# Performance work log

Hardware: AMD Instinct MI355X
Metric: run time of the kernel (lower is better)

Reference implementation:

```python
import jax, jax.numpy as jnp
import numpy as np

B, S, D = 1, 1500, 1280
H = 20
HD = D // H
FFN = 5120
EPS = 1e-5


def _layer_norm(x, w, b):
    # manual LN as in the NPU graph: mean/var/div, eps=1e-5
    mean = jnp.mean(x, axis=-1, keepdims=True)
    var = jnp.mean((x - mean) ** 2, axis=-1, keepdims=True)
    return w * ((x - mean) / jnp.sqrt(var + EPS)) + b


def setup_inputs() -> dict:
    key = jax.random.key(0)
    ks = jax.random.split(key, 16)
    r = lambda k, shp, s=1.0: jax.random.normal(k, shp, dtype=jnp.float32) * s
    return {
        "x": r(ks[0], (B, S, D)),
        "ln1_w": jax.random.uniform(ks[1], (D,), dtype=jnp.float32),
        "ln1_b": r(ks[2], (D,), 0.02),
        "ln2_w": jax.random.uniform(ks[3], (D,), dtype=jnp.float32),
        "ln2_b": r(ks[4], (D,), 0.02),
        "wq": r(ks[5], (D, D), 0.02),
        "q_bias": r(ks[6], (D,), 0.02),
        "wk": r(ks[7], (D, D), 0.02),
        "wv": r(ks[8], (D, D), 0.02),
        "v_bias": r(ks[9], (D,), 0.02),
        "wo": r(ks[10], (D, D), 0.02),
        "out_bias": r(ks[11], (D,), 0.02),
        "w_fc1": r(ks[12], (FFN, D), 0.02),
        "fc1_bias": r(ks[13], (FFN,), 0.02),
        "w_fc2": r(ks[14], (D, FFN), 0.02),
        "fc2_bias": r(ks[15], (D,), 0.02),
    }


def reference(x, ln1_w, ln1_b, ln2_w, ln2_b, wq, q_bias, wk, wv, v_bias,
              wo, out_bias, w_fc1, fc1_bias, w_fc2, fc2_bias):
    scaling = HD ** -0.5
    residual = x
    h = _layer_norm(x.reshape(B * S, D), ln1_w, ln1_b)

    # self-attention (k_proj has no bias, as in Whisper)
    q = (h @ wq.T + q_bias) * scaling            # [S, D]
    k = h @ wk.T
    v = h @ wv.T + v_bias
    q = q.reshape(S, H, HD).transpose(1, 0, 2)   # [H, S, HD]
    k = k.reshape(S, H, HD).transpose(1, 0, 2)
    v = v.reshape(S, H, HD).transpose(1, 0, 2)

    attn = jnp.einsum('hqd,hkd->hqk', q, k)      # [H, S, S]
    attn = jax.nn.softmax(attn, axis=-1)
    ctx = jnp.einsum('hqk,hkd->hqd', attn, v)    # [H, S, HD]
    ctx = ctx.transpose(1, 0, 2).reshape(S, D)
    attn_out = ctx @ wo.T + out_bias

    h = residual + attn_out.reshape(B, S, D)

    residual = h
    h2 = _layer_norm(h.reshape(B * S, D), ln2_w, ln2_b)
    h2 = jax.nn.gelu(h2 @ w_fc1.T + fc1_bias, approximate=False)
    h2 = h2 @ w_fc2.T + fc2_bias
    return residual + h2.reshape(B, S, D)
```

## Files before the change

### kernel.cpp

```cpp
#include <hip/hip_runtime.h>
#include <math.h>

typedef unsigned short u16;
typedef __attribute__((ext_vector_type(8))) short bf16x8;
typedef __attribute__((ext_vector_type(4))) float f32x4;

#define S_VALID 1500
#define S_PAD   1536
#define DMODEL  1280
#define NHEAD   20
#define HDIM    64
#define FFND    5120
#define NKV_TILES 47

__device__ __forceinline__ u16 f2bf(float f) {
  union { float f; unsigned u; } v; v.f = f;
  unsigned r = v.u + 0x7fffu + ((v.u >> 16) & 1u);
  return (u16)(r >> 16);
}

template <int N>
__device__ __forceinline__ void wait_vmcnt() {
  if constexpr (N == 8)      asm volatile("s_waitcnt vmcnt(8)"  ::: "memory");
  else if constexpr (N == 6) asm volatile("s_waitcnt vmcnt(6)"  ::: "memory");
  else if constexpr (N == 4) asm volatile("s_waitcnt vmcnt(4)"  ::: "memory");
  else                       asm volatile("s_waitcnt vmcnt(0)"  ::: "memory");
}

__global__ void k_cvt4(const float* __restrict__ s0, const float* __restrict__ s1,
                       const float* __restrict__ s2, const float* __restrict__ s3,
                       u16* __restrict__ d0, u16* __restrict__ d1,
                       u16* __restrict__ d2, u16* __restrict__ d3, int n) {
  const float* in = (blockIdx.y == 0) ? s0 : (blockIdx.y == 1) ? s1 : (blockIdx.y == 2) ? s2 : s3;
  u16* out = (blockIdx.y == 0) ? d0 : (blockIdx.y == 1) ? d1 : (blockIdx.y == 2) ? d2 : d3;
  int i = (blockIdx.x * 256 + threadIdx.x) * 4;
  if (i >= n) return;
  float4 f = *(const float4*)(in + i);
  union { u16 s[4]; uint2 v; } o;
  o.s[0] = f2bf(f.x); o.s[1] = f2bf(f.y); o.s[2] = f2bf(f.z); o.s[3] = f2bf(f.w);
  *(uint2*)(out + i) = o.v;
}
__global__ void k_cvt2(const float* __restrict__ s0, const float* __restrict__ s1,
                       u16* __restrict__ d0, u16* __restrict__ d1, int n) {
  const float* in = (blockIdx.y == 0) ? s0 : s1;
  u16* out = (blockIdx.y == 0) ? d0 : d1;
  int i = (blockIdx.x * 256 + threadIdx.x) * 4;
  if (i >= n) return;
  float4 f = *(const float4*)(in + i);
  union { u16 s[4]; uint2 v; } o;
  o.s[0] = f2bf(f.x); o.s[1] = f2bf(f.y); o.s[2] = f2bf(f.z); o.s[3] = f2bf(f.w);
  *(uint2*)(out + i) = o.v;
}

__global__ __launch_bounds__(256) void k_ln(const float* __restrict__ x,
                                            const float* __restrict__ w,
                                            const float* __restrict__ b,
                                            u16* __restrict__ out, int rows_valid) {
  int r = blockIdx.x;
  int t = threadIdx.x;
  if (r >= rows_valid) {
    for (int i = t; i < DMODEL; i += 256) out[r * DMODEL + i] = 0;
    return;
  }
  const float* xr = x + (size_t)r * DMODEL;
  float vals[5]; float s = 0.f, ss = 0.f;
#pragma unroll
  for (int j = 0; j < 5; ++j) {
    float v = xr[t + j * 256]; vals[j] = v; s += v; ss += v * v;
  }
#pragma unroll
  for (int m = 1; m < 64; m <<= 1) { s += __shfl_xor(s, m); ss += __shfl_xor(ss, m); }
  __shared__ float ps[4], pss[4];
  int lane = t & 63, wv = t >> 6;
  if (lane == 0) { ps[wv] = s; pss[wv] = ss; }
  __syncthreads();
  s = ps[0] + ps[1] + ps[2] + ps[3];
  ss = pss[0] + pss[1] + pss[2] + pss[3];
  float mean = s * (1.f / DMODEL);
  float var = ss * (1.f / DMODEL) - mean * mean;
  float rstd = rsqrtf(var + 1e-5f);
#pragma unroll
  for (int j = 0; j < 5; ++j) {
    int i = t + j * 256;
    out[r * DMODEL + i] = f2bf(w[i] * ((vals[j] - mean) * rstd) + b[i]);
  }
}

struct EpiParams {
  const float* bias;
  const float* resid;
  float* outf;
  u16* outb;
  u16* q; u16* k; u16* vt;
  const float* qb; const float* vb;
  int mvalid;
};

template <int ROWS>
__device__ __forceinline__ void stage_tile(const u16* __restrict__ g, int ld,
                                           u16* lds, int t) {
  constexpr int ITERS = ROWS * 128 / (256 * 16);
#pragma unroll
  for (int i = 0; i < ITERS; ++i) {
    int off = i * 4096 + t * 16;
    int row = off >> 7;
    int sp  = (off >> 4) & 7;
    int s   = sp ^ (row & 7);
    const u16* gp = g + row * ld + s * 8;
    u16* lp = lds + i * 2048 + ((t >> 6) << 9);
    __builtin_amdgcn_global_load_lds((const __attribute__((address_space(1))) void*)gp,
                                     (__attribute__((address_space(3))) void*)lp,
                                     16, 0, 0);
  }
}

__device__ __forceinline__ bf16x8 ld_frag(const u16* lds, int row, int kk, int lane) {
  int slot = kk * 4 + (lane >> 4);
  int sp = slot ^ (row & 7);
  return *(const bf16x8*)(lds + row * 64 + sp * 8);
}

template <int BM, int BN, int EPI>
__global__ __launch_bounds__(256) void k_gemm(const u16* __restrict__ A,
                                              const u16* __restrict__ B,
                                              int N, int K, int lda, int ldb,
                                              EpiParams ep) {
  constexpr int FM = BM / 32, FN = BN / 32;
  constexpr int LOADS = (BM + BN) / 32;
  __shared__ __align__(128) u16 lds_a[2][BM * 64];
  __shared__ __align__(128) u16 lds_b[2][BN * 64];
  const int t = threadIdx.x, lane = t & 63, wid = t >> 6;
  const int wm = wid >> 1, wn = wid & 1;

  unsigned nwg = gridDim.x * gridDim.y;
  unsigned bid = blockIdx.y * gridDim.x + blockIdx.x;
  unsigned cpx = nwg >> 3;
  bid = (bid & 7u) * cpx + (bid >> 3);
  const int bm0 = (bid % gridDim.x) * BM, bn0 = (bid / gridDim.x) * BN;

  const int l15 = lane & 15, g4 = lane >> 4;

  f32x4 acc[FM][FN] = {};
  const size_t zk = (EPI == 4) ? (size_t)blockIdx.z * K : 0;
  const u16* Ab = A + (size_t)bm0 * lda + zk;
  const u16* Bb = B + (size_t)bn0 * ldb + zk;

  auto stage = [&](int kt, int buf) {
    stage_tile<BM>(Ab + kt * 64, lda, &lds_a[buf][0], t);
    stage_tile<BN>(Bb + kt * 64, ldb, &lds_b[buf][0], t);
  };

  const int NT = K >> 6;
  stage(0, 0);
  int buf = 0;

  for (int kt = 0; kt < NT; ++kt) {
    if (kt + 1 < NT) {
      stage(kt + 1, buf ^ 1);
      wait_vmcnt<LOADS>();
    } else {
      wait_vmcnt<0>();
    }
    __builtin_amdgcn_s_barrier();
    const u16* la = &lds_a[buf][0];
    const u16* lb = &lds_b[buf][0];
#pragma unroll
    for (int kk = 0; kk < 2; ++kk) {
      bf16x8 af[FM], bfr[FN];
#pragma unroll
      for (int i = 0; i < FM; ++i) af[i]  = ld_frag(la, wm * (BM / 2) + i * 16 + l15, kk, lane);
#pragma unroll
      for (int j = 0; j < FN; ++j) bfr[j] = ld_frag(lb, wn * (BN / 2) + j * 16 + l15, kk, lane);
#pragma unroll
      for (int i = 0; i < FM; ++i)
#pragma unroll
        for (int j = 0; j < FN; ++j)
          acc[i][j] = __builtin_amdgcn_mfma_f32_16x16x32_bf16(af[i], bfr[j], acc[i][j], 0, 0, 0);
    }
    __builtin_amdgcn_s_barrier();
    buf ^= 1;
  }

#pragma unroll
  for (int i = 0; i < FM; ++i)
#pragma unroll
    for (int j = 0; j < FN; ++j) {
      int n = bn0 + wn * (BN / 2) + j * 16 + l15;
      int mbase = bm0 + wm * (BM / 2) + i * 16 + g4 * 4;
      if constexpr (EPI == 0) {
        if (n >= 2 * DMODEL) {
          int nn = n - 2 * DMODEL;
          union { u16 s[4]; uint2 v2; } pk;
#pragma unroll
          for (int r = 0; r < 4; ++r) {
            int m = mbase + r;
            float val = (m < ep.mvalid) ? (acc[i][j][r] + ep.vb[nn]) : 0.f;
            pk.s[r] = f2bf(val);
          }
          *(uint2*)(ep.vt + (size_t)nn * S_PAD + mbase) = pk.v2;
        } else {
#pragma unroll
          for (int r = 0; r < 4; ++r) {
            int m = mbase + r;
            float v = acc[i][j][r];
            if (n < DMODEL) {
              float val = (m < ep.mvalid) ? (v + ep.qb[n]) * 0.125f : 0.f;
              ep.q[m * DMODEL + n] = f2bf(val);
            } else {
              int nn = n - DMODEL;
              ep.k[m * DMODEL + nn] = f2bf(m < ep.mvalid ? v : 0.f);
            }
          }
        }
      } else {
#pragma unroll
        for (int r = 0; r < 4; ++r) {
          int m = mbase + r;
          float v = acc[i][j][r];
          if constexpr (EPI == 2) {
            float xx = v + ep.bias[n];
            float gg = 0.5f * xx * (1.f + erff(xx * 0.70710678118f));
            ep.outb[(size_t)m * N + n] = f2bf(gg);
          } else if constexpr (EPI == 4) {
            ep.outf[((size_t)blockIdx.z * S_PAD + m) * DMODEL + n] = v;
          }
        }
      }
    }
}

__global__ __launch_bounds__(256) void k_red(const float* __restrict__ p,
                                             const float* __restrict__ bias,
                                             const float* __restrict__ resid,
                                             float* __restrict__ out) {
  int idx = blockIdx.x * 256 + threadIdx.x;
  if (idx >= S_VALID * (DMODEL / 4)) return;
  int m = idx / (DMODEL / 4), n4 = (idx % (DMODEL / 4)) * 4;
  float4 a  = *(const float4*)(p + (size_t)m * DMODEL + n4);
  float4 b  = *(const float4*)(p + ((size_t)S_PAD + m) * DMODEL + n4);
  float4 rs = *(const float4*)(resid + (size_t)m * DMODEL + n4);
  float4 bb = *(const float4*)(bias + n4);
  float4 o;
  o.x = a.x + b.x + rs.x + bb.x;
  o.y = a.y + b.y + rs.y + bb.y;
  o.z = a.z + b.z + rs.z + bb.z;
  o.w = a.w + b.w + rs.w + bb.w;
  *(float4*)(out + (size_t)m * DMODEL + n4) = o;
}

__global__ __launch_bounds__(256) void k_attn(const u16* __restrict__ q,
                                              const u16* __restrict__ k,
                                              const u16* __restrict__ vt,
                                              u16* __restrict__ ctx) {
  __shared__ __align__(128) u16 kls[2][32 * 64];
  __shared__ __align__(128) u16 vls[2][32 * 64];
  const int t = threadIdx.x;
  const int lane = t & 63, wid = t >> 6;
  const int h = blockIdx.y;
  const int qbase = blockIdx.x * 64 + wid * 16;
  const int l15 = lane & 15, g = lane >> 4;

  const int srow = t >> 3;
  const int psl  = t & 7;
  const int slog = psl ^ (srow & 7);
  const int kperm = 8 * ((srow & 15) >> 2) + (srow & 3) + 4 * (srow >> 4);
  const int vd    = 2 * srow + (slog >> 2);
  const int vkoff = (slog & 3) * 8;
  const u16* ksrc = k + (size_t)kperm * DMODEL + h * HDIM + slog * 8;
  const u16* vsrc = vt + (size_t)(h * HDIM + vd) * S_PAD + vkoff;
  const int wbase = (t >> 6) << 9;

  bf16x8 qf[2];
#pragma unroll
  for (int half = 0; half < 2; ++half)
    qf[half] = *(const bf16x8*)(q + (qbase + l15) * DMODEL + h * HDIM + half * 32 + g * 8);

  auto stage = [&](int tt, int buf) {
    __builtin_amdgcn_global_load_lds(
        (const __attribute__((address_space(1))) void*)(ksrc + (size_t)tt * 32 * DMODEL),
        (__attribute__((address_space(3))) void*)(&kls[buf][0] + wbase), 16, 0, 0);
    __builtin_amdgcn_global_load_lds(
        (const __attribute__((address_space(1))) void*)(vsrc + tt * 32),
        (__attribute__((address_space(3))) void*)(&vls[buf][0] + wbase), 16, 0, 0);
  };

  stage(0, 0);
  __syncthreads();
  int buf = 0;

  float Mx = -1e30f, L = 0.f;
  f32x4 c[4] = {};

  for (int tt = 0; tt < NKV_TILES; ++tt) {
    if (tt + 1 < NKV_TILES) stage(tt + 1, buf ^ 1);
    const u16* kb = &kls[buf][0];
    const u16* vbL = &vls[buf][0];

    f32x4 sc[2];
#pragma unroll
    for (int s = 0; s < 2; ++s) {
      int row = 16 * s + l15;
      bf16x8 ka0 = *(const bf16x8*)(kb + row * 64 + ((g)     ^ (row & 7)) * 8);
      bf16x8 ka1 = *(const bf16x8*)(kb + row * 64 + ((4 + g) ^ (row & 7)) * 8);
      f32x4 z = {};
      z = __builtin_amdgcn_mfma_f32_16x16x32_bf16(ka0, qf[0], z, 0, 0, 0);
      z = __builtin_amdgcn_mfma_f32_16x16x32_bf16(ka1, qf[1], z, 0, 0, 0);
      sc[s] = z;
    }
    float pm = -1e30f;
#pragma unroll
    for (int s = 0; s < 2; ++s)
#pragma unroll
      for (int r = 0; r < 4; ++r) {
        int kg = tt * 32 + 8 * g + 4 * s + r;
        float v = (kg < S_VALID) ? sc[s][r] : -1e30f;
        sc[s][r] = v;
        pm = fmaxf(pm, v);
      }
    pm = fmaxf(pm, __shfl_xor(pm, 16));
    pm = fmaxf(pm, __shfl_xor(pm, 32));
    float Mn = fmaxf(Mx, pm);
    float fac = __expf(Mx - Mn);
    float p[8]; float rs = 0.f;
#pragma unroll
    for (int s = 0; s < 2; ++s)
#pragma unroll
      for (int r = 0; r < 4; ++r) {
        float e = __expf(sc[s][r] - Mn);
        p[4 * s + r] = e; rs += e;
      }
    rs += __shfl_xor(rs, 16);
    rs += __shfl_xor(rs, 32);
    L = L * fac + rs; Mx = Mn;

    float facr[4];
#pragma unroll
    for (int r = 0; r < 4; ++r) facr[r] = __shfl(fac, g * 20 + r);
#pragma unroll
    for (int ch = 0; ch < 4; ++ch)
#pragma unroll
      for (int r = 0; r < 4; ++r) c[ch][r] *= facr[r];

    bf16x8 pa;
#pragma unroll
    for (int j = 0; j < 8; ++j) pa[j] = (short)f2bf(p[j]);
#pragma unroll
    for (int ch = 0; ch < 4; ++ch) {
      int R = 8 * ch + (l15 >> 1);
      int sl = (l15 & 1) * 4 + g;
      bf16x8 vbf = *(const bf16x8*)(vbL + R * 64 + (sl ^ (R & 7)) * 8);
      c[ch] = __builtin_amdgcn_mfma_f32_16x16x32_bf16(pa, vbf, c[ch], 0, 0, 0);
    }
    __syncthreads();
    buf ^= 1;
  }

  float linv = 1.f / L;
  float lr[4];
#pragma unroll
  for (int r = 0; r < 4; ++r) lr[r] = __shfl(linv, g * 20 + r);
#pragma unroll
  for (int ch = 0; ch < 4; ++ch)
#pragma unroll
    for (int r = 0; r < 4; ++r) {
      int m = qbase + g * 4 + r;
      ctx[m * DMODEL + h * HDIM + ch * 16 + l15] = f2bf(c[ch][r] * lr[r]);
    }
}

extern "C" void kernel_launch(void* const* d_in, const int* in_sizes, int n_in,
                              void* d_out, int out_size, void* d_ws, size_t ws_size,
                              hipStream_t stream) {
  const float* x    = (const float*)d_in[0];
  const float* ln1w = (const float*)d_in[1];
  const float* ln1b = (const float*)d_in[2];
  const float* ln2w = (const float*)d_in[3];
  const float* ln2b = (const float*)d_in[4];
  const float* wq   = (const float*)d_in[5];
  const float* qb   = (const float*)d_in[6];
  const float* wk   = (const float*)d_in[7];
  const float* wv   = (const float*)d_in[8];
  const float* vb   = (const float*)d_in[9];
  const float* wo   = (const float*)d_in[10];
  const float* ob   = (const float*)d_in[11];
  const float* wfc1 = (const float*)d_in[12];
  const float* fb1  = (const float*)d_in[13];
  const float* wfc2 = (const float*)d_in[14];
  const float* fb2  = (const float*)d_in[15];

  char* ws = (char*)d_ws;
  size_t off = 0;
  auto alloc = [&](size_t bytes) {
    void* p = ws + off; off += (bytes + 255) & ~(size_t)255; return p;
  };
  u16*   w_qkv = (u16*)alloc((size_t)3 * DMODEL * DMODEL * 2);
  u16*   w_o   = (u16*)alloc((size_t)DMODEL * DMODEL * 2);
  u16*   w_f1  = (u16*)alloc((size_t)FFND * DMODEL * 2);
  u16*   w_f2  = (u16*)alloc((size_t)DMODEL * FFND * 2);
  u16*   hbuf  = (u16*)alloc((size_t)S_PAD * DMODEL * 2);
  u16*   qbuf  = (u16*)alloc((size_t)S_PAD * DMODEL * 2);
  u16*   kbuf  = (u16*)alloc((size_t)S_PAD * DMODEL * 2);
  u16*   vtb   = (u16*)alloc((size_t)DMODEL * S_PAD * 2);
  u16*   ctxb  = (u16*)alloc((size_t)S_PAD * DMODEL * 2);
  float* res2  = (float*)alloc((size_t)S_PAD * DMODEL * 4);
  u16*   h2buf = (u16*)alloc((size_t)S_PAD * DMODEL * 2);
  u16*   gbuf  = (u16*)alloc((size_t)S_PAD * FFND * 2);
  float* skp   = (float*)hbuf;
  (void)ws_size; (void)n_in; (void)in_sizes; (void)out_size;

  const int nDD = DMODEL * DMODEL;
  const int nF  = FFND * DMODEL;
  k_cvt4<<<dim3(nDD / 1024, 4), 256, 0, stream>>>(
      wq, wk, wv, wo, w_qkv, w_qkv + (size_t)nDD, w_qkv + (size_t)2 * nDD, w_o, nDD);
  k_cvt2<<<dim3(nF / 1024, 2), 256, 0, stream>>>(wfc1, wfc2, w_f1, w_f2, nF);

  k_ln<<<S_PAD, 256, 0, stream>>>(x, ln1w, ln1b, hbuf, S_VALID);

  {
    EpiParams ep = {};
    ep.q = qbuf; ep.k = kbuf; ep.vt = vtb; ep.qb = qb; ep.vb = vb; ep.mvalid = S_VALID;
    k_gemm<64, 64, 0><<<dim3(S_PAD / 64, 3 * DMODEL / 64), 256, 0, stream>>>(
        hbuf, w_qkv, 3 * DMODEL, DMODEL, DMODEL, DMODEL, ep);
  }

  k_attn<<<dim3(S_PAD / 64, NHEAD), 256, 0, stream>>>(qbuf, kbuf, vtb, ctxb);

  {
    EpiParams ep = {};
    ep.outf = skp; ep.mvalid = S_VALID;
    k_gemm<64, 64, 4><<<dim3(S_PAD / 64, DMODEL / 64, 2), 256, 0, stream>>>(
        ctxb, w_o, DMODEL, DMODEL / 2, DMODEL, DMODEL, ep);
  }
  k_red<<<(S_VALID * (DMODEL / 4) + 255) / 256, 256, 0, stream>>>(
      skp, ob, x, res2);

  k_ln<<<S_PAD, 256, 0, stream>>>(res2, ln2w, ln2b, h2buf, S_VALID);

  {
    EpiParams ep = {};
    ep.bias = fb1; ep.outb = gbuf; ep.mvalid = S_VALID;
    k_gemm<64, 64, 2><<<dim3(S_PAD / 64, FFND / 64), 256, 0, stream>>>(
        h2buf, w_f1, FFND, DMODEL, DMODEL, DMODEL, ep);
  }

  {
    EpiParams ep = {};
    ep.outf = skp; ep.mvalid = S_VALID;
    k_gemm<64, 64, 4><<<dim3(S_PAD / 64, DMODEL / 64, 2), 256, 0, stream>>>(
        gbuf, w_f2, DMODEL, FFND / 2, FFND, FFND, ep);
  }
  k_red<<<(S_VALID * (DMODEL / 4) + 255) / 256, 256, 0, stream>>>(
      skp, fb2, res2, (float*)d_out);
}
```

Measured before the change: 208.6 us.

## Split attention keys in two halves with a combine kernel and 64-key tiles

The attention kernel now splits the key range into two halves of 768 across a third grid dimension, doubling the block count from 480 to 960 so the GPU's compute units are better filled. Each half writes unnormalized bf16 partial outputs plus per-row max and sum, and a new combine kernel merges them with rescaling. Each iteration now processes 64 keys from two 32-key LDS subtiles, and the barrier uses explicit vmcnt waits with s_barrier in place of __syncthreads. In exchange it adds an extra launch, extra global traffic for the partials, and bf16 rounding of the unnormalized partials, and it reuses the res2 buffer as scratch.

```diff
diff --git a/kernel.cpp b/kernel.cpp
--- a/kernel.cpp
+++ b/kernel.cpp
@@ -11,12 +11,16 @@
 #define NHEAD   20
 #define HDIM    64
 #define FFND    5120
-#define NKV_TILES 47
+#define ZKEYS   768
+#define NSPLIT_TILES 12
 
 __device__ __forceinline__ u16 f2bf(float f) {
   union { float f; unsigned u; } v; v.f = f;
   unsigned r = v.u + 0x7fffu + ((v.u >> 16) & 1u);
   return (u16)(r >> 16);
+}
+__device__ __forceinline__ float bf2f(u16 h) {
+  union { unsigned u; float f; } v; v.u = ((unsigned)h) << 16; return v.f;
 }
 
 template <int N>
@@ -251,12 +255,15 @@
 __global__ __launch_bounds__(256) void k_attn(const u16* __restrict__ q,
                                               const u16* __restrict__ k,
                                               const u16* __restrict__ vt,
-                                              u16* __restrict__ ctx) {
-  __shared__ __align__(128) u16 kls[2][32 * 64];
-  __shared__ __align__(128) u16 vls[2][32 * 64];
+                                              u16* __restrict__ o0,
+                                              u16* __restrict__ o1,
+                                              float2* __restrict__ ml) {
+  __shared__ __align__(128) u16 kls[2][2][2048];
+  __shared__ __align__(128) u16 vls[2][2][2048];
   const int t = threadIdx.x;
   const int lane = t & 63, wid = t >> 6;
-  const int h = blockIdx.y;
+  const int h = blockIdx.y, z = blockIdx.z;
+  const int zb = z * ZKEYS;
   const int qbase = blockIdx.x * 64 + wid * 16;
   const int l15 = lane & 15, g = lane >> 4;
 
@@ -266,8 +273,8 @@
   const int kperm = 8 * ((srow & 15) >> 2) + (srow & 3) + 4 * (srow >> 4);
   const int vd    = 2 * srow + (slog >> 2);
   const int vkoff = (slog & 3) * 8;
-  const u16* ksrc = k + (size_t)kperm * DMODEL + h * HDIM + slog * 8;
-  const u16* vsrc = vt + (size_t)(h * HDIM + vd) * S_PAD + vkoff;
+  const u16* kbasep = k + (size_t)kperm * DMODEL + h * HDIM + slog * 8;
+  const u16* vbasep = vt + (size_t)(h * HDIM + vd) * S_PAD + vkoff;
   const int wbase = (t >> 6) << 9;
 
   bf16x8 qf[2];
@@ -276,59 +283,73 @@
     qf[half] = *(const bf16x8*)(q + (qbase + l15) * DMODEL + h * HDIM + half * 32 + g * 8);
 
   auto stage = [&](int tt, int buf) {
-    __builtin_amdgcn_global_load_lds(
-        (const __attribute__((address_space(1))) void*)(ksrc + (size_t)tt * 32 * DMODEL),
-        (__attribute__((address_space(3))) void*)(&kls[buf][0] + wbase), 16, 0, 0);
-    __builtin_amdgcn_global_load_lds(
-        (const __attribute__((address_space(1))) void*)(vsrc + tt * 32),
-        (__attribute__((address_space(3))) void*)(&vls[buf][0] + wbase), 16, 0, 0);
+#pragma unroll
+    for (int u = 0; u < 2; ++u) {
+      int keyoff = zb + tt * 64 + u * 32;
+      __builtin_amdgcn_global_load_lds(
+          (const __attribute__((address_space(1))) void*)(kbasep + (size_t)keyoff * DMODEL),
+          (__attribute__((address_space(3))) void*)(&kls[buf][u][0] + wbase), 16, 0, 0);
+      __builtin_amdgcn_global_load_lds(
+          (const __attribute__((address_space(1))) void*)(vbasep + keyoff),
+          (__attribute__((address_space(3))) void*)(&vls[buf][u][0] + wbase), 16, 0, 0);
+    }
   };
 
   stage(0, 0);
-  __syncthreads();
   int buf = 0;
 
   float Mx = -1e30f, L = 0.f;
   f32x4 c[4] = {};
 
-  for (int tt = 0; tt < NKV_TILES; ++tt) {
-    if (tt + 1 < NKV_TILES) stage(tt + 1, buf ^ 1);
-    const u16* kb = &kls[buf][0];
-    const u16* vbL = &vls[buf][0];
-
-    f32x4 sc[2];
-#pragma unroll
-    for (int s = 0; s < 2; ++s) {
-      int row = 16 * s + l15;
-      bf16x8 ka0 = *(const bf16x8*)(kb + row * 64 + ((g)     ^ (row & 7)) * 8);
-      bf16x8 ka1 = *(const bf16x8*)(kb + row * 64 + ((4 + g) ^ (row & 7)) * 8);
-      f32x4 z = {};
-      z = __builtin_amdgcn_mfma_f32_16x16x32_bf16(ka0, qf[0], z, 0, 0, 0);
-      z = __builtin_amdgcn_mfma_f32_16x16x32_bf16(ka1, qf[1], z, 0, 0, 0);
-      sc[s] = z;
-    }
+  for (int tt = 0; tt < NSPLIT_TILES; ++tt) {
+    if (tt + 1 < NSPLIT_TILES) {
+      stage(tt + 1, buf ^ 1);
+      wait_vmcnt<4>();
+    } else {
+      wait_vmcnt<0>();
+    }
+    __builtin_amdgcn_s_barrier();
+
+    f32x4 sc[2][2];
+#pragma unroll
+    for (int u = 0; u < 2; ++u)
+#pragma unroll
+      for (int s = 0; s < 2; ++s) {
+        int row = 16 * s + l15;
+        const u16* kb = &kls[buf][u][0];
+        bf16x8 ka0 = *(const bf16x8*)(kb + row * 64 + ((g)     ^ (row & 7)) * 8);
+        bf16x8 ka1 = *(const bf16x8*)(kb + row * 64 + ((4 + g) ^ (row & 7)) * 8);
+        f32x4 zz = {};
+        zz = __builtin_amdgcn_mfma_f32_16x16x32_bf16(ka0, qf[0], zz, 0, 0, 0);
+        zz = __builtin_amdgcn_mfma_f32_16x16x32_bf16(ka1, qf[1], zz, 0, 0, 0);
+        sc[u][s] = zz;
+      }
     float pm = -1e30f;
 #pragma unroll
-    for (int s = 0; s < 2; ++s)
-#pragma unroll
-      for (int r = 0; r < 4; ++r) {
-        int kg = tt * 32 + 8 * g + 4 * s + r;
-        float v = (kg < S_VALID) ? sc[s][r] : -1e30f;
-        sc[s][r] = v;
-        pm = fmaxf(pm, v);
-      }
+    for (int u = 0; u < 2; ++u)
+#pragma unroll
+      for (int s = 0; s < 2; ++s)
+#pragma unroll
+        for (int r = 0; r < 4; ++r) {
+          int kg = zb + tt * 64 + u * 32 + 8 * g + 4 * s + r;
+          float v = (kg < S_VALID) ? sc[u][s][r] : -1e30f;
+          sc[u][s][r] = v;
+          pm = fmaxf(pm, v);
+        }
     pm = fmaxf(pm, __shfl_xor(pm, 16));
     pm = fmaxf(pm, __shfl_xor(pm, 32));
     float Mn = fmaxf(Mx, pm);
     float fac = __expf(Mx - Mn);
-    float p[8]; float rs = 0.f;
-#pragma unroll
-    for (int s = 0; s < 2; ++s)
-#pragma unroll
-      for (int r = 0; r < 4; ++r) {
-        float e = __expf(sc[s][r] - Mn);
-        p[4 * s + r] = e; rs += e;
-      }
+    float p[2][8]; float rs = 0.f;
+#pragma unroll
+    for (int u = 0; u < 2; ++u)
+#pragma unroll
+      for (int s = 0; s < 2; ++s)
+#pragma unroll
+        for (int r = 0; r < 4; ++r) {
+          float e = __expf(sc[u][s][r] - Mn);
+          p[u][4 * s + r] = e; rs += e;
+        }
     rs += __shfl_xor(rs, 16);
     rs += __shfl_xor(rs, 32);
     L = L * fac + rs; Mx = Mn;
@@ -341,31 +362,57 @@
 #pragma unroll
       for (int r = 0; r < 4; ++r) c[ch][r] *= facr[r];
 
-    bf16x8 pa;
-#pragma unroll
-    for (int j = 0; j < 8; ++j) pa[j] = (short)f2bf(p[j]);
+    bf16x8 pa[2];
+#pragma unroll
+    for (int u = 0; u < 2; ++u)
+#pragma unroll
+      for (int j = 0; j < 8; ++j) pa[u][j] = (short)f2bf(p[u][j]);
 #pragma unroll
     for (int ch = 0; ch < 4; ++ch) {
       int R = 8 * ch + (l15 >> 1);
       int sl = (l15 & 1) * 4 + g;
-      bf16x8 vbf = *(const bf16x8*)(vbL + R * 64 + (sl ^ (R & 7)) * 8);
-      c[ch] = __builtin_amdgcn_mfma_f32_16x16x32_bf16(pa, vbf, c[ch], 0, 0, 0);
-    }
-    __syncthreads();
+#pragma unroll
+      for (int u = 0; u < 2; ++u) {
+        bf16x8 vbf = *(const bf16x8*)(&vls[buf][u][0] + R * 64 + (sl ^ (R & 7)) * 8);
+        c[ch] = __builtin_amdgcn_mfma_f32_16x16x32_bf16(pa[u], vbf, c[ch], 0, 0, 0);
+      }
+    }
+    __builtin_amdgcn_s_barrier();
     buf ^= 1;
   }
 
-  float linv = 1.f / L;
-  float lr[4];
-#pragma unroll
-  for (int r = 0; r < 4; ++r) lr[r] = __shfl(linv, g * 20 + r);
+  u16* op = z ? o1 : o0;
+  if (g == 0) ml[(size_t)(z * NHEAD + h) * S_PAD + qbase + l15] = make_float2(Mx, L);
 #pragma unroll
   for (int ch = 0; ch < 4; ++ch)
 #pragma unroll
     for (int r = 0; r < 4; ++r) {
       int m = qbase + g * 4 + r;
-      ctx[m * DMODEL + h * HDIM + ch * 16 + l15] = f2bf(c[ch][r] * lr[r]);
-    }
+      op[(size_t)m * DMODEL + h * HDIM + ch * 16 + l15] = f2bf(c[ch][r]);
+    }
+}
+
+__global__ __launch_bounds__(256) void k_comb(u16* __restrict__ o0,
+                                              const u16* __restrict__ o1,
+                                              const float2* __restrict__ ml) {
+  int idx = blockIdx.x * 256 + threadIdx.x;
+  if (idx >= S_VALID * (DMODEL / 4)) return;
+  int m = idx / (DMODEL / 4);
+  int d = (idx % (DMODEL / 4)) * 4;
+  int h = d >> 6;
+  float2 a = ml[(size_t)h * S_PAD + m];
+  float2 b = ml[(size_t)(NHEAD + h) * S_PAD + m];
+  float M = fmaxf(a.x, b.x);
+  float w0 = __expf(a.x - M), w1 = __expf(b.x - M);
+  float inv = 1.f / (w0 * a.y + w1 * b.y);
+  w0 *= inv; w1 *= inv;
+  union { u16 s[4]; uint2 v; } A, B, O;
+  A.v = *(const uint2*)(o0 + (size_t)m * DMODEL + d);
+  B.v = *(const uint2*)(o1 + (size_t)m * DMODEL + d);
+#pragma unroll
+  for (int j = 0; j < 4; ++j)
+    O.s[j] = f2bf(w0 * bf2f(A.s[j]) + w1 * bf2f(B.s[j]));
+  *(uint2*)(o0 + (size_t)m * DMODEL + d) = O.v;
 }
 
 extern "C" void kernel_launch(void* const* d_in, const int* in_sizes, int n_in,
@@ -406,6 +453,8 @@
   u16*   h2buf = (u16*)alloc((size_t)S_PAD * DMODEL * 2);
   u16*   gbuf  = (u16*)alloc((size_t)S_PAD * FFND * 2);
   float* skp   = (float*)hbuf;
+  u16*    opart1 = (u16*)res2;
+  float2* mlbuf  = (float2*)((char*)res2 + (size_t)S_PAD * DMODEL * 2);
   (void)ws_size; (void)n_in; (void)in_sizes; (void)out_size;
 
   const int nDD = DMODEL * DMODEL;
@@ -423,7 +472,10 @@
         hbuf, w_qkv, 3 * DMODEL, DMODEL, DMODEL, DMODEL, ep);
   }
 
-  k_attn<<<dim3(S_PAD / 64, NHEAD), 256, 0, stream>>>(qbuf, kbuf, vtb, ctxb);
+  k_attn<<<dim3(S_PAD / 64, NHEAD, 2), 256, 0, stream>>>(
+      qbuf, kbuf, vtb, ctxb, opart1, mlbuf);
+  k_comb<<<(S_VALID * (DMODEL / 4) + 255) / 256, 256, 0, stream>>>(
+      ctxb, opart1, mlbuf);
 
   {
     EpiParams ep = {};
```

After: 196.3 us. -5.9%, faster.
